# Performance work log

Measured on AMD Instinct MI355X. Metric: run time of the kernel, lower is better.

The kernel has to match this reference:

```python
import jax, jax.numpy as jnp
import numpy as np

I = 512   # input_size
H = 512   # hidden_size
Z = 0.1   # zoneout rate (eval-mode deterministic blend)
S = 128   # number of segments
B = 64    # batch


def setup_inputs() -> dict:
    rng = np.random.default_rng(0)
    durs = rng.integers(4, 13, size=(S, B)).astype(np.int64)  # [S, B], all >= 1
    T = int(durs.sum(0).max())
    key = jax.random.key(0)
    k0, k1, k2, k3, k4 = jax.random.split(key, 5)
    k = 1.0 / np.sqrt(H)
    x = jax.random.normal(k0, (T, B, I), jnp.float32)
    W_ih = jax.random.uniform(k1, (4 * H, I), jnp.float32, -k, k)
    W_hh = jax.random.uniform(k2, (4 * H, H), jnp.float32, -k, k)
    b_ih = jax.random.uniform(k3, (4 * H,), jnp.float32, -k, k)
    b_hh = jax.random.uniform(k4, (4 * H,), jnp.float32, -k, k)
    return {"x": x, "durs": jnp.asarray(durs), "W_ih": W_ih, "W_hh": W_hh,
            "b_ih": b_ih, "b_hh": b_hh}


def _duration_masks(durs, T):
    # durs: [S, B] -> per-batch segment-end (reset) frame indices and masks
    durs_bs = durs.T                                   # [B, S]
    reset_idx = jnp.cumsum(durs_bs, axis=1) - 1        # [B, S] last frame of each segment
    mel_lengths = jnp.sum(durs_bs, axis=1)             # [B]
    t = jnp.arange(T)
    reset_mask = jnp.any(t[None, :, None] == reset_idx[:, None, :], axis=-1)  # [B, T]
    valid = t[None, :] < mel_lengths[:, None]          # [B, T] frames within mel length
    retain = (~reset_mask) & valid                     # state kept where not reset/pad
    return reset_idx, retain.T, valid.T                # retain/valid as [T, B]


def reference(x, durs, W_ih, W_hh, b_ih, b_hh):
    T, Bb, _ = x.shape
    reset_idx, retain, valid = _duration_masks(durs, T)
    # Precompute the input contribution to the gates for all timesteps (one big GEMM)
    xg = jnp.einsum('tbi,gi->tbg', x, W_ih) + b_ih + b_hh   # [T, B, 4H]
    retain_f = retain.astype(x.dtype)                       # [T, B]

    def step(carry, inp):
        h, c = carry
        xg_t, retain_t = inp
        gates = xg_t + h @ W_hh.T                           # [B, 4H]
        i, f, g, o = jnp.split(gates, 4, axis=-1)           # torch LSTMCell order i,f,g,o
        i = jax.nn.sigmoid(i); f = jax.nn.sigmoid(f); o = jax.nn.sigmoid(o)
        g = jnp.tanh(g)
        c_new = f * c + i * g
        h_new = o * jnp.tanh(c_new)
        # eval-mode zoneout: deterministic blend with previous state
        h_z = Z * h + (1.0 - Z) * h_new
        c_z = Z * c + (1.0 - Z) * c_new
        m = retain_t[:, None]                               # zero state at segment resets / padding
        return (h_z * m, c_z * m), h_z

    h0 = jnp.zeros((Bb, H), x.dtype)
    (h, c), outputs = jax.lax.scan(step, (h0, h0), (xg, retain_f))
    outputs = outputs * valid[:, :, None].astype(outputs.dtype)  # [T, B, H]
    # segout: hidden state at each segment's last frame -> [B, S, H]
    segout = jnp.take_along_axis(outputs.transpose(1, 0, 2), reset_idx[:, :, None], axis=1)
    return outputs, h, c, segout
```

## Files before the change

### kernel.cpp

```cpp
#include <hip/hip_runtime.h>
#include <hip/hip_fp16.h>

#define IDIM 512
#define HDIM 512
#define NGATE 2048
#define SEGS 128
#define BATCH 64
#define ZK 0.1f

typedef _Float16 f16;
typedef _Float16 f16x8 __attribute__((ext_vector_type(8)));
typedef float f32x4 __attribute__((ext_vector_type(4)));

__device__ __forceinline__ void gload16(const void* g, void* l) {
  __builtin_amdgcn_global_load_lds((const __attribute__((address_space(1))) void*)g,
                                   (__attribute__((address_space(3))) void*)l, 16, 0, 0);
}
__device__ __forceinline__ float sigmoidf_(float x) { return 1.0f / (1.0f + __expf(-x)); }
__device__ __forceinline__ float tanhf_(float x) { return 2.0f / (1.0f + __expf(-2.0f * x)) - 1.0f; }

__global__ void prep_kernel(const int* __restrict__ durs, int4* __restrict__ meta,
                            int* __restrict__ Mk, int* __restrict__ mel) {
  __shared__ int hist[16];
  __shared__ int cur[16];
  int tid = threadIdx.x;
  if (tid < 16) hist[tid] = 0;
  __syncthreads();
  int b = tid;
  for (int s = 0; s < SEGS; ++s) {
    int d = durs[s * BATCH + b] & 15;
    atomicAdd(&hist[d], 1);
  }
  __syncthreads();
  if (tid == 0) {
    int run = 0;
    for (int d = 15; d >= 0; --d) { cur[d] = run; run += hist[d]; }
    for (int kk = 0; kk < 12; ++kk) Mk[kk] = cur[kk];
  }
  __syncthreads();
  int run = 0;
  for (int s = 0; s < SEGS; ++s) {
    int d = durs[s * BATCH + b] & 15;
    int pos = atomicAdd(&cur[d], 1);
    meta[pos] = make_int4(run, b, s, d);
    run += d;
  }
  mel[b] = run;
}

__global__ void wprep_kernel(const float* __restrict__ Wih, const float* __restrict__ Whh,
                             const float* __restrict__ bih, const float* __restrict__ bhh,
                             f16* __restrict__ Wc, float* __restrict__ biasp) {
  int n = blockIdx.x;
  int G = n >> 6, q = (n >> 4) & 3, r = n & 15;
  int j = G * 16 + r;
  int orig = q * 512 + j;
  for (int kk = threadIdx.x; kk < 1024; kk += blockDim.x) {
    float v = (kk < 512) ? Wih[(size_t)orig * 512 + kk] : Whh[(size_t)orig * 512 + kk - 512];
    Wc[(size_t)n * 1024 + kk] = (f16)v;
  }
  if (threadIdx.x == 0) biasp[n] = bih[orig] + bhh[orig];
}

__global__ void xconv_kernel(const float* __restrict__ x, f16* __restrict__ xh, long n8) {
  long i = (long)blockIdx.x * blockDim.x + threadIdx.x;
  long stride = (long)gridDim.x * blockDim.x;
  for (; i < n8; i += stride) {
    const float4* p = (const float4*)(x + i * 8);
    float4 a = p[0], bv = p[1];
    f16x8 o;
    o[0] = (f16)a.x;  o[1] = (f16)a.y;  o[2] = (f16)a.z;  o[3] = (f16)a.w;
    o[4] = (f16)bv.x; o[5] = (f16)bv.y; o[6] = (f16)bv.z; o[7] = (f16)bv.w;
    *(f16x8*)(xh + i * 8) = o;
  }
}

__global__ void zero_kernel(float* __restrict__ out, const int* __restrict__ mel, int T) {
  int bid = blockIdx.x;
  int tb = T * BATCH;
  if (bid < tb) {
    int t = bid / BATCH, b = bid - t * BATCH;
    if (t < mel[b]) return;
    float4* p = (float4*)(out + (size_t)bid * HDIM);
    p[threadIdx.x] = make_float4(0.f, 0.f, 0.f, 0.f);
  } else {
    int e = bid - tb;
    float4* p = (float4*)(out + (size_t)tb * HDIM + (size_t)e * HDIM);
    p[threadIdx.x] = make_float4(0.f, 0.f, 0.f, 0.f);
  }
}

template <bool FIRST>
__global__ __launch_bounds__(512, 1)
void step256_kernel(const f16* __restrict__ xh, const f16* __restrict__ Wc,
                    const float* __restrict__ biasp,
                    const f16* __restrict__ hprev, f16* __restrict__ hnext,
                    float* __restrict__ cst,
                    const int4* __restrict__ meta, const int* __restrict__ Mk,
                    float* __restrict__ out, int T, int k) {
  const int mk = Mk[k];
  const int nbx = gridDim.x;
  const int nwg = nbx * gridDim.y;
  const int orig = blockIdx.y * nbx + blockIdx.x;
  const int cpx = nwg >> 3;
  const int swz = (orig & 7) * cpx + (orig >> 3);
  const int by = swz / nbx, bx = swz - by * nbx;
  const int m0 = by * 256;
  if (m0 >= mk) return;
  const int n0 = bx * 256;

  __shared__ __align__(16) f16 As[2][256][64];
  __shared__ __align__(16) f16 Bs[2][256][64];
  __shared__ int4 metaS[256];

  const int tid = threadIdx.x;
  const int lane = tid & 63;
  const int w = tid >> 6;
  const int wr = w >> 2;
  const int wc = w & 3;
  const int lr = lane & 15;
  const int lk = lane >> 4;

  if (tid < 256) metaS[tid] = meta[m0 + tid];

  const int swzc = (((lane & 7) ^ ((lane >> 3) & 7)) << 3);
  size_t xoff[4];
  int ra4[4];
#pragma unroll
  for (int o = 0; o < 4; ++o) {
    int trow = o * 64 + w * 8 + (lane >> 3);
    int r = m0 + trow;
    int ra = (r < mk) ? r : 0;
    int4 mt = meta[ra];
    xoff[o] = ((size_t)(mt.x + k) * BATCH + mt.y) * IDIM + swzc;
    ra4[o] = ra;
  }

  auto stageA = [&](int o, int kb, int slot) {
    const f16* src;
    if (FIRST || kb < 8) src = xh + xoff[o] + kb * 64;
    else src = hprev + (size_t)ra4[o] * HDIM + (kb - 8) * 64 + swzc;
    gload16(src, &As[slot][o * 64 + w * 8][0]);
  };
  auto stageB = [&](int o, int kb, int slot) {
    int trow = o * 64 + w * 8 + (lane >> 3);
    gload16(Wc + (size_t)(n0 + trow) * 1024 + (size_t)kb * 64 + swzc,
            &Bs[slot][o * 64 + w * 8][0]);
  };

  auto lda = [&](int slot, int h, int f, int ks) -> f16x8 {
    int row = wr * 128 + h * 64 + f * 16 + lr;
    int ch = (((ks * 4 + lk) ^ (lr & 7)) << 3);
    return *(const f16x8*)&As[slot][row][ch];
  };
  auto ldb = [&](int slot, int q, int ks) -> f16x8 {
    int row = wc * 64 + q * 16 + lr;
    int ch = (((ks * 4 + lk) ^ (lr & 7)) << 3);
    return *(const f16x8*)&Bs[slot][row][ch];
  };

  f32x4 acc[8][4];
#pragma unroll
  for (int a = 0; a < 8; ++a)
#pragma unroll
    for (int bb = 0; bb < 4; ++bb) acc[a][bb] = (f32x4){0.f, 0.f, 0.f, 0.f};

  const int KB = FIRST ? 8 : 16;

#pragma unroll
  for (int o = 0; o < 4; ++o) stageA(o, 0, 0);
#pragma unroll
  for (int o = 0; o < 4; ++o) stageB(o, 0, 0);
#pragma unroll
  for (int o = 0; o < 4; ++o) stageA(o, 1, 1);
#pragma unroll
  for (int o = 0; o < 4; ++o) stageB(o, 1, 1);
  asm volatile("s_waitcnt vmcnt(8)" ::: "memory");
  __builtin_amdgcn_s_barrier();

  f16x8 aF[4][2], bF[4][2];

  for (int kt = 0; kt < KB; ++kt) {
    const int s = kt & 1;
    const bool st1 = (kt + 1 < KB);
    const bool st2 = (kt + 2 < KB);

#pragma unroll
    for (int f = 0; f < 4; ++f)
#pragma unroll
      for (int ks = 0; ks < 2; ++ks) aF[f][ks] = lda(s, 0, f, ks);
#pragma unroll
    for (int q = 0; q < 4; ++q)
#pragma unroll
      for (int ks = 0; ks < 2; ++ks) bF[q][ks] = ldb(s, q, ks);
    __builtin_amdgcn_s_barrier();
    __builtin_amdgcn_s_setprio(1);
#pragma unroll
    for (int f = 0; f < 4; ++f)
#pragma unroll
      for (int fn = 0; fn < 2; ++fn)
#pragma unroll
        for (int ks = 0; ks < 2; ++ks)
          acc[f][fn] = __builtin_amdgcn_mfma_f32_16x16x32_f16(aF[f][ks], bF[fn][ks], acc[f][fn], 0, 0, 0);
    __builtin_amdgcn_s_setprio(0);
    __builtin_amdgcn_s_barrier();

    if (st2) {
#pragma unroll
      for (int o = 0; o < 4; ++o) stageB(o, kt + 2, s);
    }
    __builtin_amdgcn_s_barrier();
    __builtin_amdgcn_s_setprio(1);
#pragma unroll
    for (int f = 0; f < 4; ++f)
#pragma unroll
      for (int fn = 2; fn < 4; ++fn)
#pragma unroll
        for (int ks = 0; ks < 2; ++ks)
          acc[f][fn] = __builtin_amdgcn_mfma_f32_16x16x32_f16(aF[f][ks], bF[fn][ks], acc[f][fn], 0, 0, 0);
    __builtin_amdgcn_s_setprio(0);
    __builtin_amdgcn_s_barrier();

#pragma unroll
    for (int f = 0; f < 4; ++f)
#pragma unroll
      for (int ks = 0; ks < 2; ++ks) aF[f][ks] = lda(s, 1, f, ks);
    if (st2) { stageA(0, kt + 2, s); stageA(2, kt + 2, s); }
    __builtin_amdgcn_s_barrier();
    __builtin_amdgcn_s_setprio(1);
#pragma unroll
    for (int f = 0; f < 4; ++f)
#pragma unroll
      for (int fn = 0; fn < 2; ++fn)
#pragma unroll
        for (int ks = 0; ks < 2; ++ks)
          acc[4 + f][fn] = __builtin_amdgcn_mfma_f32_16x16x32_f16(aF[f][ks], bF[fn][ks], acc[4 + f][fn], 0, 0, 0);
    __builtin_amdgcn_s_setprio(0);
    __builtin_amdgcn_s_barrier();

    if (st2) { stageA(1, kt + 2, s); stageA(3, kt + 2, s); }
    __builtin_amdgcn_s_setprio(1);
#pragma unroll
    for (int f = 0; f < 4; ++f)
#pragma unroll
      for (int fn = 2; fn < 4; ++fn)
#pragma unroll
        for (int ks = 0; ks < 2; ++ks)
          acc[4 + f][fn] = __builtin_amdgcn_mfma_f32_16x16x32_f16(aF[f][ks], bF[fn][ks], acc[4 + f][fn], 0, 0, 0);
    __builtin_amdgcn_s_setprio(0);
    if (st2) {
      asm volatile("s_waitcnt vmcnt(8)" ::: "memory");
    } else if (st1) {
      asm volatile("s_waitcnt vmcnt(0)" ::: "memory");
    }
    __builtin_amdgcn_s_barrier();
  }

  float bq[4];
#pragma unroll
  for (int q = 0; q < 4; ++q) bq[q] = biasp[n0 + wc * 64 + q * 16 + lr];
  const int j = ((n0 + wc * 64) >> 6) * 16 + lr;
  const size_t segoff = (size_t)T * BATCH * HDIM + (size_t)2 * BATCH * HDIM;

#pragma unroll
  for (int fm = 0; fm < 8; ++fm) {
#pragma unroll
    for (int reg = 0; reg < 4; ++reg) {
      int m = m0 + wr * 128 + fm * 16 + ((lane >> 4) << 2) + reg;
      if (m >= mk) continue;
      int4 mt = metaS[m - m0];
      float gi = acc[fm][0][reg] + bq[0];
      float gf = acc[fm][1][reg] + bq[1];
      float gg = acc[fm][2][reg] + bq[2];
      float go = acc[fm][3][reg] + bq[3];
      float iv = sigmoidf_(gi), fv = sigmoidf_(gf);
      float gv = tanhf_(gg), ov = sigmoidf_(go);
      float cp, hp;
      if (FIRST) { cp = 0.f; hp = 0.f; }
      else {
        cp = cst[(size_t)m * HDIM + j];
        hp = (float)hprev[(size_t)m * HDIM + j];
      }
      float cn = fv * cp + iv * gv;
      float hn = ov * tanhf_(cn);
      float hz = ZK * hp + (1.f - ZK) * hn;
      float cz = ZK * cp + (1.f - ZK) * cn;
      out[((size_t)(mt.x + k) * BATCH + mt.y) * HDIM + j] = hz;
      if (k == mt.w - 1) {
        out[segoff + ((size_t)mt.y * SEGS + mt.z) * HDIM + j] = hz;
      } else {
        hnext[(size_t)m * HDIM + j] = (f16)hz;
        cst[(size_t)m * HDIM + j] = cz;
      }
    }
  }
}

template <bool FIRST>
__global__ void step_kernel(const f16* __restrict__ xh, const f16* __restrict__ Wc,
                            const float* __restrict__ biasp,
                            const f16* __restrict__ hprev, f16* __restrict__ hnext,
                            float* __restrict__ cst,
                            const int4* __restrict__ meta, const int* __restrict__ Mk,
                            float* __restrict__ out, int T, int k) {
  const int mk = Mk[k];
  const int m0 = blockIdx.y * 128;
  if (m0 >= mk) return;
  const int n0 = blockIdx.x * 128;

  __shared__ __align__(16) f16 At[128][64];
  __shared__ __align__(16) f16 Bt[128][64];
  __shared__ int4 metaS[128];

  const int tid = threadIdx.x;
  const int lane = tid & 63;
  const int w = tid >> 6;
  const int wr = w >> 1, wc = w & 1;

  if (tid < 128) metaS[tid] = meta[m0 + tid];

  const f16* xsrc[4];
  const f16* hsrc[4];
  const f16* wsrc[4];
#pragma unroll
  for (int i = 0; i < 4; ++i) {
    int r = m0 + w * 32 + i * 8 + (lane >> 3);
    int ra = (r < mk) ? r : 0;
    int4 mt = meta[ra];
    xsrc[i] = xh + ((size_t)(mt.x + k) * BATCH + mt.y) * IDIM;
    hsrc[i] = hprev + (size_t)ra * HDIM;
    wsrc[i] = Wc + (size_t)(n0 + w * 32 + i * 8 + (lane >> 3)) * 1024;
  }
  const int koff = (lane & 7) * 8;

  f32x4 acc[4][4];
#pragma unroll
  for (int a = 0; a < 4; ++a)
#pragma unroll
    for (int bb = 0; bb < 4; ++bb) acc[a][bb] = (f32x4){0.f, 0.f, 0.f, 0.f};

  const int KB = FIRST ? 8 : 16;
  for (int kb = 0; kb < KB; ++kb) {
    __syncthreads();
#pragma unroll
    for (int i = 0; i < 4; ++i) {
      const f16* s;
      if (FIRST) s = xsrc[i] + kb * 64 + koff;
      else       s = (kb < 8) ? (xsrc[i] + kb * 64 + koff) : (hsrc[i] + (kb - 8) * 64 + koff);
      gload16(s, &At[w * 32 + i * 8][0]);
    }
#pragma unroll
    for (int i = 0; i < 4; ++i) gload16(wsrc[i] + kb * 64 + koff, &Bt[w * 32 + i * 8][0]);
    __syncthreads();

    const int lr = lane & 15;
    const int lk = (lane >> 4) * 8;
#pragma unroll
    for (int ks = 0; ks < 2; ++ks) {
      f16x8 af[4], bfr[4];
#pragma unroll
      for (int f = 0; f < 4; ++f) af[f] = *(const f16x8*)&At[wr * 64 + f * 16 + lr][ks * 32 + lk];
#pragma unroll
      for (int f = 0; f < 4; ++f) bfr[f] = *(const f16x8*)&Bt[wc * 64 + f * 16 + lr][ks * 32 + lk];
#pragma unroll
      for (int fm = 0; fm < 4; ++fm)
#pragma unroll
        for (int fn = 0; fn < 4; ++fn)
          acc[fm][fn] = __builtin_amdgcn_mfma_f32_16x16x32_f16(af[fm], bfr[fn], acc[fm][fn], 0, 0, 0);
    }
  }

  const int r15 = lane & 15;
  float bq[4];
#pragma unroll
  for (int q = 0; q < 4; ++q) bq[q] = biasp[n0 + wc * 64 + q * 16 + r15];
  const int j = ((n0 + wc * 64) >> 6) * 16 + r15;
  const size_t segoff = (size_t)T * BATCH * HDIM + (size_t)2 * BATCH * HDIM;

#pragma unroll
  for (int fm = 0; fm < 4; ++fm) {
#pragma unroll
    for (int reg = 0; reg < 4; ++reg) {
      int m = m0 + wr * 64 + fm * 16 + ((lane >> 4) << 2) + reg;
      if (m >= mk) continue;
      int4 mt = metaS[m - m0];
      float gi = acc[fm][0][reg] + bq[0];
      float gf = acc[fm][1][reg] + bq[1];
      float gg = acc[fm][2][reg] + bq[2];
      float go = acc[fm][3][reg] + bq[3];
      float iv = sigmoidf_(gi), fv = sigmoidf_(gf);
      float gv = tanhf_(gg), ov = sigmoidf_(go);
      float cp, hp;
      if (FIRST) { cp = 0.f; hp = 0.f; }
      else {
        cp = cst[(size_t)m * HDIM + j];
        hp = (float)hprev[(size_t)m * HDIM + j];
      }
      float cn = fv * cp + iv * gv;
      float hn = ov * tanhf_(cn);
      float hz = ZK * hp + (1.f - ZK) * hn;
      float cz = ZK * cp + (1.f - ZK) * cn;
      out[((size_t)(mt.x + k) * BATCH + mt.y) * HDIM + j] = hz;
      if (k == mt.w - 1) {
        out[segoff + ((size_t)mt.y * SEGS + mt.z) * HDIM + j] = hz;
      } else {
        hnext[(size_t)m * HDIM + j] = (f16)hz;
        cst[(size_t)m * HDIM + j] = cz;
      }
    }
  }
}

extern "C" void kernel_launch(void* const* d_in, const int* in_sizes, int n_in,
                              void* d_out, int out_size, void* d_ws, size_t ws_size,
                              hipStream_t stream) {
  const float* x = (const float*)d_in[0];
  const int* durs = (const int*)d_in[1];
  const float* Wih = (const float*)d_in[2];
  const float* Whh = (const float*)d_in[3];
  const float* bih = (const float*)d_in[4];
  const float* bhh = (const float*)d_in[5];
  float* out = (float*)d_out;
  const int T = in_sizes[0] / (BATCH * IDIM);

  char* ws = (char*)d_ws;
  size_t off = 0;
  auto alloc = [&](size_t bytes) {
    void* p = ws + off;
    off = (off + bytes + 255) & ~(size_t)255;
    return p;
  };
  f16* xh     = (f16*)alloc((size_t)T * BATCH * IDIM * 2);
  f16* Wc     = (f16*)alloc((size_t)NGATE * 1024 * 2);
  float* biasp= (float*)alloc((size_t)NGATE * 4);
  f16* hst0   = (f16*)alloc((size_t)SEGS * BATCH * HDIM * 2);
  f16* hst1   = (f16*)alloc((size_t)SEGS * BATCH * HDIM * 2);
  float* cst  = (float*)alloc((size_t)SEGS * BATCH * HDIM * 4);
  int4* meta  = (int4*)alloc((size_t)SEGS * BATCH * 16);
  int* Mk     = (int*)alloc(64);
  int* mel    = (int*)alloc(64);

  prep_kernel<<<1, 64, 0, stream>>>(durs, meta, Mk, mel);
  wprep_kernel<<<NGATE, 256, 0, stream>>>(Wih, Whh, bih, bhh, Wc, biasp);
  long n8 = (long)T * BATCH * IDIM / 8;
  xconv_kernel<<<2048, 256, 0, stream>>>(x, xh, n8);
  zero_kernel<<<T * BATCH + 128, 128, 0, stream>>>(out, mel, T);

  dim3 hgrid(8, 32);
  step256_kernel<true><<<hgrid, 512, 0, stream>>>(xh, Wc, biasp, hst0, hst1, cst, meta, Mk, out, T, 0);
  for (int k = 1; k < 8; ++k) {
    f16* hp = (k & 1) ? hst1 : hst0;
    f16* hn = (k & 1) ? hst0 : hst1;
    step256_kernel<false><<<hgrid, 512, 0, stream>>>(xh, Wc, biasp, hp, hn, cst, meta, Mk, out, T, k);
  }
  dim3 sgrid(16, 64);
  for (int k = 8; k < 12; ++k) {
    f16* hp = (k & 1) ? hst1 : hst0;
    f16* hn = (k & 1) ? hst0 : hst1;
    step_kernel<false><<<sgrid, 256, 0, stream>>>(xh, Wc, biasp, hp, hn, cst, meta, Mk, out, T, k);
  }
}
```

Before: 654.7 us.

## Fuse per-step LSTM launches into one persistent cooperative kernel with grid sync

Replaces the 12 separate step launches, which mixed 256-tile and 128-tile kernels, with a single cooperative persistent kernel of 256 blocks. The kernel loops over the 12 frame positions and calls grid.sync between them, and it always uses 256x256 tiles with a simple row-major tile mapping instead of the XCD swizzle. The zero kernel also becomes grid-stride with a fixed grid. The goal is to remove launch gaps and tail idle time between dependent steps. In exchange, the later small steps now use large tiles, which can leave many blocks idle, and the swizzle that spread tiles across XCDs for cache locality is gone.

```diff
diff --git a/kernel.cpp b/kernel.cpp
--- a/kernel.cpp
+++ b/kernel.cpp
@@ -1,5 +1,8 @@
 #include <hip/hip_runtime.h>
 #include <hip/hip_fp16.h>
+#include <hip/hip_cooperative_groups.h>
+
+namespace cg = cooperative_groups;
 
 #define IDIM 512
 #define HDIM 512
@@ -27,10 +30,7 @@
   if (tid < 16) hist[tid] = 0;
   __syncthreads();
   int b = tid;
-  for (int s = 0; s < SEGS; ++s) {
-    int d = durs[s * BATCH + b] & 15;
-    atomicAdd(&hist[d], 1);
-  }
+  for (int s = 0; s < SEGS; ++s) atomicAdd(&hist[durs[s * BATCH + b] & 15], 1);
   __syncthreads();
   if (tid == 0) {
     int run = 0;
@@ -75,44 +75,37 @@
   }
 }
 
-__global__ void zero_kernel(float* __restrict__ out, const int* __restrict__ mel, int T) {
-  int bid = blockIdx.x;
+__global__ void zero_kernel(float* __restrict__ out, const int* __restrict__ mel,
+                            int T, int total) {
   int tb = T * BATCH;
-  if (bid < tb) {
-    int t = bid / BATCH, b = bid - t * BATCH;
-    if (t < mel[b]) return;
-    float4* p = (float4*)(out + (size_t)bid * HDIM);
-    p[threadIdx.x] = make_float4(0.f, 0.f, 0.f, 0.f);
-  } else {
-    int e = bid - tb;
-    float4* p = (float4*)(out + (size_t)tb * HDIM + (size_t)e * HDIM);
-    p[threadIdx.x] = make_float4(0.f, 0.f, 0.f, 0.f);
-  }
-}
-
-template <bool FIRST>
+  for (int bid = blockIdx.x; bid < total; bid += gridDim.x) {
+    if (bid < tb) {
+      int t = bid / BATCH, b = bid - t * BATCH;
+      if (t < mel[b]) continue;
+      float4* p = (float4*)(out + (size_t)bid * HDIM);
+      p[threadIdx.x] = make_float4(0.f, 0.f, 0.f, 0.f);
+    } else {
+      int e = bid - tb;
+      float4* p = (float4*)(out + (size_t)tb * HDIM + (size_t)e * HDIM);
+      p[threadIdx.x] = make_float4(0.f, 0.f, 0.f, 0.f);
+    }
+  }
+}
+
 __global__ __launch_bounds__(512, 1)
-void step256_kernel(const f16* __restrict__ xh, const f16* __restrict__ Wc,
+void persist_kernel(const f16* __restrict__ xh, const f16* __restrict__ Wc,
                     const float* __restrict__ biasp,
-                    const f16* __restrict__ hprev, f16* __restrict__ hnext,
+                    f16* __restrict__ hst0, f16* __restrict__ hst1,
                     float* __restrict__ cst,
                     const int4* __restrict__ meta, const int* __restrict__ Mk,
-                    float* __restrict__ out, int T, int k) {
-  const int mk = Mk[k];
-  const int nbx = gridDim.x;
-  const int nwg = nbx * gridDim.y;
-  const int orig = blockIdx.y * nbx + blockIdx.x;
-  const int cpx = nwg >> 3;
-  const int swz = (orig & 7) * cpx + (orig >> 3);
-  const int by = swz / nbx, bx = swz - by * nbx;
-  const int m0 = by * 256;
-  if (m0 >= mk) return;
-  const int n0 = bx * 256;
+                    float* __restrict__ out, int T) {
+  cg::grid_group grid = cg::this_grid();
 
   __shared__ __align__(16) f16 As[2][256][64];
   __shared__ __align__(16) f16 Bs[2][256][64];
   __shared__ int4 metaS[256];
 
+  const int bid = blockIdx.x;
   const int tid = threadIdx.x;
   const int lane = tid & 63;
   const int w = tid >> 6;
@@ -120,294 +113,194 @@
   const int wc = w & 3;
   const int lr = lane & 15;
   const int lk = lane >> 4;
-
-  if (tid < 256) metaS[tid] = meta[m0 + tid];
-
   const int swzc = (((lane & 7) ^ ((lane >> 3) & 7)) << 3);
-  size_t xoff[4];
-  int ra4[4];
-#pragma unroll
-  for (int o = 0; o < 4; ++o) {
-    int trow = o * 64 + w * 8 + (lane >> 3);
-    int r = m0 + trow;
-    int ra = (r < mk) ? r : 0;
-    int4 mt = meta[ra];
-    xoff[o] = ((size_t)(mt.x + k) * BATCH + mt.y) * IDIM + swzc;
-    ra4[o] = ra;
-  }
-
-  auto stageA = [&](int o, int kb, int slot) {
-    const f16* src;
-    if (FIRST || kb < 8) src = xh + xoff[o] + kb * 64;
-    else src = hprev + (size_t)ra4[o] * HDIM + (kb - 8) * 64 + swzc;
-    gload16(src, &As[slot][o * 64 + w * 8][0]);
-  };
-  auto stageB = [&](int o, int kb, int slot) {
-    int trow = o * 64 + w * 8 + (lane >> 3);
-    gload16(Wc + (size_t)(n0 + trow) * 1024 + (size_t)kb * 64 + swzc,
-            &Bs[slot][o * 64 + w * 8][0]);
-  };
-
-  auto lda = [&](int slot, int h, int f, int ks) -> f16x8 {
-    int row = wr * 128 + h * 64 + f * 16 + lr;
-    int ch = (((ks * 4 + lk) ^ (lr & 7)) << 3);
-    return *(const f16x8*)&As[slot][row][ch];
-  };
-  auto ldb = [&](int slot, int q, int ks) -> f16x8 {
-    int row = wc * 64 + q * 16 + lr;
-    int ch = (((ks * 4 + lk) ^ (lr & 7)) << 3);
-    return *(const f16x8*)&Bs[slot][row][ch];
-  };
-
-  f32x4 acc[8][4];
-#pragma unroll
-  for (int a = 0; a < 8; ++a)
-#pragma unroll
-    for (int bb = 0; bb < 4; ++bb) acc[a][bb] = (f32x4){0.f, 0.f, 0.f, 0.f};
-
-  const int KB = FIRST ? 8 : 16;
-
-#pragma unroll
-  for (int o = 0; o < 4; ++o) stageA(o, 0, 0);
-#pragma unroll
-  for (int o = 0; o < 4; ++o) stageB(o, 0, 0);
-#pragma unroll
-  for (int o = 0; o < 4; ++o) stageA(o, 1, 1);
-#pragma unroll
-  for (int o = 0; o < 4; ++o) stageB(o, 1, 1);
-  asm volatile("s_waitcnt vmcnt(8)" ::: "memory");
-  __builtin_amdgcn_s_barrier();
-
-  f16x8 aF[4][2], bF[4][2];
-
-  for (int kt = 0; kt < KB; ++kt) {
-    const int s = kt & 1;
-    const bool st1 = (kt + 1 < KB);
-    const bool st2 = (kt + 2 < KB);
-
-#pragma unroll
-    for (int f = 0; f < 4; ++f)
-#pragma unroll
-      for (int ks = 0; ks < 2; ++ks) aF[f][ks] = lda(s, 0, f, ks);
-#pragma unroll
-    for (int q = 0; q < 4; ++q)
-#pragma unroll
-      for (int ks = 0; ks < 2; ++ks) bF[q][ks] = ldb(s, q, ks);
-    __builtin_amdgcn_s_barrier();
-    __builtin_amdgcn_s_setprio(1);
-#pragma unroll
-    for (int f = 0; f < 4; ++f)
-#pragma unroll
-      for (int fn = 0; fn < 2; ++fn)
-#pragma unroll
-        for (int ks = 0; ks < 2; ++ks)
-          acc[f][fn] = __builtin_amdgcn_mfma_f32_16x16x32_f16(aF[f][ks], bF[fn][ks], acc[f][fn], 0, 0, 0);
-    __builtin_amdgcn_s_setprio(0);
-    __builtin_amdgcn_s_barrier();
-
-    if (st2) {
-#pragma unroll
-      for (int o = 0; o < 4; ++o) stageB(o, kt + 2, s);
-    }
-    __builtin_amdgcn_s_barrier();
-    __builtin_amdgcn_s_setprio(1);
-#pragma unroll
-    for (int f = 0; f < 4; ++f)
-#pragma unroll
-      for (int fn = 2; fn < 4; ++fn)
-#pragma unroll
-        for (int ks = 0; ks < 2; ++ks)
-          acc[f][fn] = __builtin_amdgcn_mfma_f32_16x16x32_f16(aF[f][ks], bF[fn][ks], acc[f][fn], 0, 0, 0);
-    __builtin_amdgcn_s_setprio(0);
-    __builtin_amdgcn_s_barrier();
-
-#pragma unroll
-    for (int f = 0; f < 4; ++f)
-#pragma unroll
-      for (int ks = 0; ks < 2; ++ks) aF[f][ks] = lda(s, 1, f, ks);
-    if (st2) { stageA(0, kt + 2, s); stageA(2, kt + 2, s); }
-    __builtin_amdgcn_s_barrier();
-    __builtin_amdgcn_s_setprio(1);
-#pragma unroll
-    for (int f = 0; f < 4; ++f)
-#pragma unroll
-      for (int fn = 0; fn < 2; ++fn)
-#pragma unroll
-        for (int ks = 0; ks < 2; ++ks)
-          acc[4 + f][fn] = __builtin_amdgcn_mfma_f32_16x16x32_f16(aF[f][ks], bF[fn][ks], acc[4 + f][fn], 0, 0, 0);
-    __builtin_amdgcn_s_setprio(0);
-    __builtin_amdgcn_s_barrier();
-
-    if (st2) { stageA(1, kt + 2, s); stageA(3, kt + 2, s); }
-    __builtin_amdgcn_s_setprio(1);
-#pragma unroll
-    for (int f = 0; f < 4; ++f)
-#pragma unroll
-      for (int fn = 2; fn < 4; ++fn)
-#pragma unroll
-        for (int ks = 0; ks < 2; ++ks)
-          acc[4 + f][fn] = __builtin_amdgcn_mfma_f32_16x16x32_f16(aF[f][ks], bF[fn][ks], acc[4 + f][fn], 0, 0, 0);
-    __builtin_amdgcn_s_setprio(0);
-    if (st2) {
+  const size_t segoff = (size_t)T * BATCH * HDIM + (size_t)2 * BATCH * HDIM;
+
+  for (int k = 0; k < 12; ++k) {
+    const int mk = Mk[k];
+    const int npan = (mk + 255) >> 8;
+    const int ntiles = npan * 8;
+    const f16* hprev = (k & 1) ? hst1 : hst0;
+    f16* hnext = (k & 1) ? hst0 : hst1;
+
+    if (bid < ntiles) {
+      const int by = bid >> 3, bx = bid & 7;
+      const int m0 = by * 256;
+      const int n0 = bx * 256;
+
+      if (tid < 256) metaS[tid] = meta[m0 + tid];
+
+      size_t xoff[4];
+      int ra4[4];
+#pragma unroll
+      for (int o = 0; o < 4; ++o) {
+        int trow = o * 64 + w * 8 + (lane >> 3);
+        int r = m0 + trow;
+        int ra = (r < mk) ? r : 0;
+        int4 mt = meta[ra];
+        xoff[o] = ((size_t)(mt.x + k) * BATCH + mt.y) * IDIM + swzc;
+        ra4[o] = ra;
+      }
+
+      auto stageA = [&](int o, int kb, int slot) {
+        const f16* src;
+        if (k == 0 || kb < 8) src = xh + xoff[o] + kb * 64;
+        else src = hprev + (size_t)ra4[o] * HDIM + (kb - 8) * 64 + swzc;
+        gload16(src, &As[slot][o * 64 + w * 8][0]);
+      };
+      auto stageB = [&](int o, int kb, int slot) {
+        int trow = o * 64 + w * 8 + (lane >> 3);
+        gload16(Wc + (size_t)(n0 + trow) * 1024 + (size_t)kb * 64 + swzc,
+                &Bs[slot][o * 64 + w * 8][0]);
+      };
+      auto lda = [&](int slot, int h, int f, int ks) -> f16x8 {
+        int row = wr * 128 + h * 64 + f * 16 + lr;
+        int ch = (((ks * 4 + lk) ^ (lr & 7)) << 3);
+        return *(const f16x8*)&As[slot][row][ch];
+      };
+      auto ldb = [&](int slot, int q, int ks) -> f16x8 {
+        int row = wc * 64 + q * 16 + lr;
+        int ch = (((ks * 4 + lk) ^ (lr & 7)) << 3);
+        return *(const f16x8*)&Bs[slot][row][ch];
+      };
+
+      f32x4 acc[8][4];
+#pragma unroll
+      for (int a = 0; a < 8; ++a)
+#pragma unroll
+        for (int bb = 0; bb < 4; ++bb) acc[a][bb] = (f32x4){0.f, 0.f, 0.f, 0.f};
+
+      const int KB = (k == 0) ? 8 : 16;
+
+#pragma unroll
+      for (int o = 0; o < 4; ++o) stageA(o, 0, 0);
+#pragma unroll
+      for (int o = 0; o < 4; ++o) stageB(o, 0, 0);
+#pragma unroll
+      for (int o = 0; o < 4; ++o) stageA(o, 1, 1);
+#pragma unroll
+      for (int o = 0; o < 4; ++o) stageB(o, 1, 1);
       asm volatile("s_waitcnt vmcnt(8)" ::: "memory");
-    } else if (st1) {
-      asm volatile("s_waitcnt vmcnt(0)" ::: "memory");
-    }
-    __builtin_amdgcn_s_barrier();
-  }
-
-  float bq[4];
-#pragma unroll
-  for (int q = 0; q < 4; ++q) bq[q] = biasp[n0 + wc * 64 + q * 16 + lr];
-  const int j = ((n0 + wc * 64) >> 6) * 16 + lr;
-  const size_t segoff = (size_t)T * BATCH * HDIM + (size_t)2 * BATCH * HDIM;
-
-#pragma unroll
-  for (int fm = 0; fm < 8; ++fm) {
-#pragma unroll
-    for (int reg = 0; reg < 4; ++reg) {
-      int m = m0 + wr * 128 + fm * 16 + ((lane >> 4) << 2) + reg;
-      if (m >= mk) continue;
-      int4 mt = metaS[m - m0];
-      float gi = acc[fm][0][reg] + bq[0];
-      float gf = acc[fm][1][reg] + bq[1];
-      float gg = acc[fm][2][reg] + bq[2];
-      float go = acc[fm][3][reg] + bq[3];
-      float iv = sigmoidf_(gi), fv = sigmoidf_(gf);
-      float gv = tanhf_(gg), ov = sigmoidf_(go);
-      float cp, hp;
-      if (FIRST) { cp = 0.f; hp = 0.f; }
-      else {
-        cp = cst[(size_t)m * HDIM + j];
-        hp = (float)hprev[(size_t)m * HDIM + j];
+      __builtin_amdgcn_s_barrier();
+
+      f16x8 aF[4][2], bF[4][2];
+
+      for (int kt = 0; kt < KB; ++kt) {
+        const int s = kt & 1;
+        const bool st1 = (kt + 1 < KB);
+        const bool st2 = (kt + 2 < KB);
+
+#pragma unroll
+        for (int f = 0; f < 4; ++f)
+#pragma unroll
+          for (int ks = 0; ks < 2; ++ks) aF[f][ks] = lda(s, 0, f, ks);
+#pragma unroll
+        for (int q = 0; q < 4; ++q)
+#pragma unroll
+          for (int ks = 0; ks < 2; ++ks) bF[q][ks] = ldb(s, q, ks);
+        __builtin_amdgcn_s_barrier();
+        __builtin_amdgcn_s_setprio(1);
+#pragma unroll
+        for (int f = 0; f < 4; ++f)
+#pragma unroll
+          for (int fn = 0; fn < 2; ++fn)
+#pragma unroll
+            for (int ks = 0; ks < 2; ++ks)
+              acc[f][fn] = __builtin_amdgcn_mfma_f32_16x16x32_f16(aF[f][ks], bF[fn][ks], acc[f][fn], 0, 0, 0);
+        __builtin_amdgcn_s_setprio(0);
+        __builtin_amdgcn_s_barrier();
+
+        if (st2) {
+#pragma unroll
+          for (int o = 0; o < 4; ++o) stageB(o, kt + 2, s);
+        }
+        __builtin_amdgcn_s_barrier();
+        __builtin_amdgcn_s_setprio(1);
+#pragma unroll
+        for (int f = 0; f < 4; ++f)
+#pragma unroll
+          for (int fn = 2; fn < 4; ++fn)
+#pragma unroll
+            for (int ks = 0; ks < 2; ++ks)
+              acc[f][fn] = __builtin_amdgcn_mfma_f32_16x16x32_f16(aF[f][ks], bF[fn][ks], acc[f][fn], 0, 0, 0);
+        __builtin_amdgcn_s_setprio(0);
+        __builtin_amdgcn_s_barrier();
+
+#pragma unroll
+        for (int f = 0; f < 4; ++f)
+#pragma unroll
+          for (int ks = 0; ks < 2; ++ks) aF[f][ks] = lda(s, 1, f, ks);
+        if (st2) { stageA(0, kt + 2, s); stageA(2, kt + 2, s); }
+        __builtin_amdgcn_s_barrier();
+        __builtin_amdgcn_s_setprio(1);
+#pragma unroll
+        for (int f = 0; f < 4; ++f)
+#pragma unroll
+          for (int fn = 0; fn < 2; ++fn)
+#pragma unroll
+            for (int ks = 0; ks < 2; ++ks)
+              acc[4 + f][fn] = __builtin_amdgcn_mfma_f32_16x16x32_f16(aF[f][ks], bF[fn][ks], acc[4 + f][fn], 0, 0, 0);
+        __builtin_amdgcn_s_setprio(0);
+        __builtin_amdgcn_s_barrier();
+
+        if (st2) { stageA(1, kt + 2, s); stageA(3, kt + 2, s); }
+        __builtin_amdgcn_s_setprio(1);
+#pragma unroll
+        for (int f = 0; f < 4; ++f)
+#pragma unroll
+          for (int fn = 2; fn < 4; ++fn)
+#pragma unroll
+            for (int ks = 0; ks < 2; ++ks)
+              acc[4 + f][fn] = __builtin_amdgcn_mfma_f32_16x16x32_f16(aF[f][ks], bF[fn][ks], acc[4 + f][fn], 0, 0, 0);
+        __builtin_amdgcn_s_setprio(0);
+        if (st2) {
+          asm volatile("s_waitcnt vmcnt(8)" ::: "memory");
+        } else if (st1) {
+          asm volatile("s_waitcnt vmcnt(0)" ::: "memory");
+        }
+        __builtin_amdgcn_s_barrier();
       }
-      float cn = fv * cp + iv * gv;
-      float hn = ov * tanhf_(cn);
-      float hz = ZK * hp + (1.f - ZK) * hn;
-      float cz = ZK * cp + (1.f - ZK) * cn;
-      out[((size_t)(mt.x + k) * BATCH + mt.y) * HDIM + j] = hz;
-      if (k == mt.w - 1) {
-        out[segoff + ((size_t)mt.y * SEGS + mt.z) * HDIM + j] = hz;
-      } else {
-        hnext[(size_t)m * HDIM + j] = (f16)hz;
-        cst[(size_t)m * HDIM + j] = cz;
+
+      float bq[4];
+#pragma unroll
+      for (int q = 0; q < 4; ++q) bq[q] = biasp[n0 + wc * 64 + q * 16 + lr];
+      const int j = ((n0 + wc * 64) >> 6) * 16 + lr;
+
+#pragma unroll
+      for (int fm = 0; fm < 8; ++fm) {
+#pragma unroll
+        for (int reg = 0; reg < 4; ++reg) {
+          int m = m0 + wr * 128 + fm * 16 + ((lane >> 4) << 2) + reg;
+          if (m >= mk) continue;
+          int4 mt = metaS[m - m0];
+          float gi = acc[fm][0][reg] + bq[0];
+          float gf = acc[fm][1][reg] + bq[1];
+          float gg = acc[fm][2][reg] + bq[2];
+          float go = acc[fm][3][reg] + bq[3];
+          float iv = sigmoidf_(gi), fv = sigmoidf_(gf);
+          float gv = tanhf_(gg), ov = sigmoidf_(go);
+          float cp, hp;
+          if (k == 0) { cp = 0.f; hp = 0.f; }
+          else {
+            cp = cst[(size_t)m * HDIM + j];
+            hp = (float)hprev[(size_t)m * HDIM + j];
+          }
+          float cn = fv * cp + iv * gv;
+          float hn = ov * tanhf_(cn);
+          float hz = ZK * hp + (1.f - ZK) * hn;
+          float cz = ZK * cp + (1.f - ZK) * cn;
+          out[((size_t)(mt.x + k) * BATCH + mt.y) * HDIM + j] = hz;
+          if (k == mt.w - 1) {
+            out[segoff + ((size_t)mt.y * SEGS + mt.z) * HDIM + j] = hz;
+          } else {
+            hnext[(size_t)m * HDIM + j] = (f16)hz;
+            cst[(size_t)m * HDIM + j] = cz;
+          }
+        }
       }
     }
-  }
-}
-
-template <bool FIRST>
-__global__ void step_kernel(const f16* __restrict__ xh, const f16* __restrict__ Wc,
-                            const float* __restrict__ biasp,
-                            const f16* __restrict__ hprev, f16* __restrict__ hnext,
-                            float* __restrict__ cst,
-                            const int4* __restrict__ meta, const int* __restrict__ Mk,
-                            float* __restrict__ out, int T, int k) {
-  const int mk = Mk[k];
-  const int m0 = blockIdx.y * 128;
-  if (m0 >= mk) return;
-  const int n0 = blockIdx.x * 128;
-
-  __shared__ __align__(16) f16 At[128][64];
-  __shared__ __align__(16) f16 Bt[128][64];
-  __shared__ int4 metaS[128];
-
-  const int tid = threadIdx.x;
-  const int lane = tid & 63;
-  const int w = tid >> 6;
-  const int wr = w >> 1, wc = w & 1;
-
-  if (tid < 128) metaS[tid] = meta[m0 + tid];
-
-  const f16* xsrc[4];
-  const f16* hsrc[4];
-  const f16* wsrc[4];
-#pragma unroll
-  for (int i = 0; i < 4; ++i) {
-    int r = m0 + w * 32 + i * 8 + (lane >> 3);
-    int ra = (r < mk) ? r : 0;
-    int4 mt = meta[ra];
-    xsrc[i] = xh + ((size_t)(mt.x + k) * BATCH + mt.y) * IDIM;
-    hsrc[i] = hprev + (size_t)ra * HDIM;
-    wsrc[i] = Wc + (size_t)(n0 + w * 32 + i * 8 + (lane >> 3)) * 1024;
-  }
-  const int koff = (lane & 7) * 8;
-
-  f32x4 acc[4][4];
-#pragma unroll
-  for (int a = 0; a < 4; ++a)
-#pragma unroll
-    for (int bb = 0; bb < 4; ++bb) acc[a][bb] = (f32x4){0.f, 0.f, 0.f, 0.f};
-
-  const int KB = FIRST ? 8 : 16;
-  for (int kb = 0; kb < KB; ++kb) {
-    __syncthreads();
-#pragma unroll
-    for (int i = 0; i < 4; ++i) {
-      const f16* s;
-      if (FIRST) s = xsrc[i] + kb * 64 + koff;
-      else       s = (kb < 8) ? (xsrc[i] + kb * 64 + koff) : (hsrc[i] + (kb - 8) * 64 + koff);
-      gload16(s, &At[w * 32 + i * 8][0]);
-    }
-#pragma unroll
-    for (int i = 0; i < 4; ++i) gload16(wsrc[i] + kb * 64 + koff, &Bt[w * 32 + i * 8][0]);
-    __syncthreads();
-
-    const int lr = lane & 15;
-    const int lk = (lane >> 4) * 8;
-#pragma unroll
-    for (int ks = 0; ks < 2; ++ks) {
-      f16x8 af[4], bfr[4];
-#pragma unroll
-      for (int f = 0; f < 4; ++f) af[f] = *(const f16x8*)&At[wr * 64 + f * 16 + lr][ks * 32 + lk];
-#pragma unroll
-      for (int f = 0; f < 4; ++f) bfr[f] = *(const f16x8*)&Bt[wc * 64 + f * 16 + lr][ks * 32 + lk];
-#pragma unroll
-      for (int fm = 0; fm < 4; ++fm)
-#pragma unroll
-        for (int fn = 0; fn < 4; ++fn)
-          acc[fm][fn] = __builtin_amdgcn_mfma_f32_16x16x32_f16(af[fm], bfr[fn], acc[fm][fn], 0, 0, 0);
-    }
-  }
-
-  const int r15 = lane & 15;
-  float bq[4];
-#pragma unroll
-  for (int q = 0; q < 4; ++q) bq[q] = biasp[n0 + wc * 64 + q * 16 + r15];
-  const int j = ((n0 + wc * 64) >> 6) * 16 + r15;
-  const size_t segoff = (size_t)T * BATCH * HDIM + (size_t)2 * BATCH * HDIM;
-
-#pragma unroll
-  for (int fm = 0; fm < 4; ++fm) {
-#pragma unroll
-    for (int reg = 0; reg < 4; ++reg) {
-      int m = m0 + wr * 64 + fm * 16 + ((lane >> 4) << 2) + reg;
-      if (m >= mk) continue;
-      int4 mt = metaS[m - m0];
-      float gi = acc[fm][0][reg] + bq[0];
-      float gf = acc[fm][1][reg] + bq[1];
-      float gg = acc[fm][2][reg] + bq[2];
-      float go = acc[fm][3][reg] + bq[3];
-      float iv = sigmoidf_(gi), fv = sigmoidf_(gf);
-      float gv = tanhf_(gg), ov = sigmoidf_(go);
-      float cp, hp;
-      if (FIRST) { cp = 0.f; hp = 0.f; }
-      else {
-        cp = cst[(size_t)m * HDIM + j];
-        hp = (float)hprev[(size_t)m * HDIM + j];
-      }
-      float cn = fv * cp + iv * gv;
-      float hn = ov * tanhf_(cn);
-      float hz = ZK * hp + (1.f - ZK) * hn;
-      float cz = ZK * cp + (1.f - ZK) * cn;
-      out[((size_t)(mt.x + k) * BATCH + mt.y) * HDIM + j] = hz;
-      if (k == mt.w - 1) {
-        out[segoff + ((size_t)mt.y * SEGS + mt.z) * HDIM + j] = hz;
-      } else {
-        hnext[(size_t)m * HDIM + j] = (f16)hz;
-        cst[(size_t)m * HDIM + j] = cz;
-      }
-    }
+
+    if (k < 11) grid.sync();
   }
 }
 
@@ -421,7 +314,7 @@
   const float* bih = (const float*)d_in[4];
   const float* bhh = (const float*)d_in[5];
   float* out = (float*)d_out;
-  const int T = in_sizes[0] / (BATCH * IDIM);
+  int T = in_sizes[0] / (BATCH * IDIM);
 
   char* ws = (char*)d_ws;
   size_t off = 0;
@@ -444,19 +337,10 @@
   wprep_kernel<<<NGATE, 256, 0, stream>>>(Wih, Whh, bih, bhh, Wc, biasp);
   long n8 = (long)T * BATCH * IDIM / 8;
   xconv_kernel<<<2048, 256, 0, stream>>>(x, xh, n8);
-  zero_kernel<<<T * BATCH + 128, 128, 0, stream>>>(out, mel, T);
-
-  dim3 hgrid(8, 32);
-  step256_kernel<true><<<hgrid, 512, 0, stream>>>(xh, Wc, biasp, hst0, hst1, cst, meta, Mk, out, T, 0);
-  for (int k = 1; k < 8; ++k) {
-    f16* hp = (k & 1) ? hst1 : hst0;
-    f16* hn = (k & 1) ? hst0 : hst1;
-    step256_kernel<false><<<hgrid, 512, 0, stream>>>(xh, Wc, biasp, hp, hn, cst, meta, Mk, out, T, k);
-  }
-  dim3 sgrid(16, 64);
-  for (int k = 8; k < 12; ++k) {
-    f16* hp = (k & 1) ? hst1 : hst0;
-    f16* hn = (k & 1) ? hst0 : hst1;
-    step_kernel<false><<<sgrid, 256, 0, stream>>>(xh, Wc, biasp, hp, hn, cst, meta, Mk, out, T, k);
-  }
-}
+  zero_kernel<<<2048, 128, 0, stream>>>(out, mel, T, T * BATCH + 128);
+
+  void* kargs[] = {(void*)&xh, (void*)&Wc, (void*)&biasp, (void*)&hst0, (void*)&hst1,
+                   (void*)&cst, (void*)&meta, (void*)&Mk, (void*)&out, (void*)&T};
+  hipLaunchCooperativeKernel((const void*)persist_kernel, dim3(256), dim3(512),
+                             kargs, 0, stream);
+}
```

After: 1.708 ms. +160.9%, slower.

## Restructure step GEMM main loop into two-tile unrolled pipeline with fragment prefetch

Applied to the files above, without the earlier changes.

Unrolls the step256 main loop over two K-tiles per iteration. It splits the A and B LDS fragment reads into quarters that are prefetched one MFMA block ahead, and reorders the staging of the next tiles with finer vmcnt waits, so LDS reads and global loads overlap more with MFMA work. The zero kernel also becomes a grid-stride loop with a fixed 2048-block grid instead of one block per row. In exchange the kernel holds more live fragment registers and depends on a more fragile wait and barrier schedule.

```diff
diff --git a/kernel.cpp b/kernel.cpp
--- a/kernel.cpp
+++ b/kernel.cpp
@@ -27,10 +27,7 @@
   if (tid < 16) hist[tid] = 0;
   __syncthreads();
   int b = tid;
-  for (int s = 0; s < SEGS; ++s) {
-    int d = durs[s * BATCH + b] & 15;
-    atomicAdd(&hist[d], 1);
-  }
+  for (int s = 0; s < SEGS; ++s) atomicAdd(&hist[durs[s * BATCH + b] & 15], 1);
   __syncthreads();
   if (tid == 0) {
     int run = 0;
@@ -75,18 +72,20 @@
   }
 }
 
-__global__ void zero_kernel(float* __restrict__ out, const int* __restrict__ mel, int T) {
-  int bid = blockIdx.x;
+__global__ void zero_kernel(float* __restrict__ out, const int* __restrict__ mel,
+                            int T, int total) {
   int tb = T * BATCH;
-  if (bid < tb) {
-    int t = bid / BATCH, b = bid - t * BATCH;
-    if (t < mel[b]) return;
-    float4* p = (float4*)(out + (size_t)bid * HDIM);
-    p[threadIdx.x] = make_float4(0.f, 0.f, 0.f, 0.f);
-  } else {
-    int e = bid - tb;
-    float4* p = (float4*)(out + (size_t)tb * HDIM + (size_t)e * HDIM);
-    p[threadIdx.x] = make_float4(0.f, 0.f, 0.f, 0.f);
+  for (int bid = blockIdx.x; bid < total; bid += gridDim.x) {
+    if (bid < tb) {
+      int t = bid / BATCH, b = bid - t * BATCH;
+      if (t < mel[b]) continue;
+      float4* p = (float4*)(out + (size_t)bid * HDIM);
+      p[threadIdx.x] = make_float4(0.f, 0.f, 0.f, 0.f);
+    } else {
+      int e = bid - tb;
+      float4* p = (float4*)(out + (size_t)tb * HDIM + (size_t)e * HDIM);
+      p[threadIdx.x] = make_float4(0.f, 0.f, 0.f, 0.f);
+    }
   }
 }
 
@@ -100,10 +99,8 @@
                     float* __restrict__ out, int T, int k) {
   const int mk = Mk[k];
   const int nbx = gridDim.x;
-  const int nwg = nbx * gridDim.y;
   const int orig = blockIdx.y * nbx + blockIdx.x;
-  const int cpx = nwg >> 3;
-  const int swz = (orig & 7) * cpx + (orig >> 3);
+  const int swz = (orig & 7) * 32 + (orig >> 3);
   const int by = swz / nbx, bx = swz - by * nbx;
   const int m0 = by * 256;
   if (m0 >= mk) return;
@@ -147,7 +144,6 @@
     gload16(Wc + (size_t)(n0 + trow) * 1024 + (size_t)kb * 64 + swzc,
             &Bs[slot][o * 64 + w * 8][0]);
   };
-
   auto lda = [&](int slot, int h, int f, int ks) -> f16x8 {
     int row = wr * 128 + h * 64 + f * 16 + lr;
     int ch = (((ks * 4 + lk) ^ (lr & 7)) << 3);
@@ -166,6 +162,7 @@
     for (int bb = 0; bb < 4; ++bb) acc[a][bb] = (f32x4){0.f, 0.f, 0.f, 0.f};
 
   const int KB = FIRST ? 8 : 16;
+  const int NITER = KB >> 1;
 
 #pragma unroll
   for (int o = 0; o < 4; ++o) stageA(o, 0, 0);
@@ -178,83 +175,118 @@
   asm volatile("s_waitcnt vmcnt(8)" ::: "memory");
   __builtin_amdgcn_s_barrier();
 
-  f16x8 aF[4][2], bF[4][2];
-
-  for (int kt = 0; kt < KB; ++kt) {
-    const int s = kt & 1;
-    const bool st1 = (kt + 1 < KB);
-    const bool st2 = (kt + 2 < KB);
+  f16x8 aF0[4][2], aF1[4][2], aN0[4][2], aN1[4][2];
+  f16x8 bA[2][2], bB[2][2], bC[2][2], bD[2][2];
+
+#pragma unroll
+  for (int f = 0; f < 4; ++f)
+#pragma unroll
+    for (int ks = 0; ks < 2; ++ks) aF0[f][ks] = lda(0, 0, f, ks);
+#pragma unroll
+  for (int q = 0; q < 2; ++q)
+#pragma unroll
+    for (int ks = 0; ks < 2; ++ks) bA[q][ks] = ldb(0, q, ks);
+
+#define MFMA_Q(ACC_R, ACC_C, AFR, BFR)                                              \
+  __builtin_amdgcn_s_setprio(1);                                                    \
+  _Pragma("unroll") for (int f = 0; f < 4; ++f)                                     \
+    _Pragma("unroll") for (int q = 0; q < 2; ++q)                                   \
+      _Pragma("unroll") for (int ks = 0; ks < 2; ++ks)                              \
+        acc[ACC_R + f][ACC_C + q] =                                                 \
+            __builtin_amdgcn_mfma_f32_16x16x32_f16(AFR[f][ks], BFR[q][ks],          \
+                                                   acc[ACC_R + f][ACC_C + q], 0, 0, 0); \
+  __builtin_amdgcn_s_setprio(0);
+
+  for (int i = 0; i < NITER; ++i) {
+    const int kt0 = 2 * i;
+    const bool st = (i + 1 < NITER);
+
+#pragma unroll
+    for (int q = 0; q < 2; ++q)
+#pragma unroll
+      for (int ks = 0; ks < 2; ++ks) bB[q][ks] = ldb(0, q + 2, ks);
+    __builtin_amdgcn_s_barrier();
+    MFMA_Q(0, 0, aF0, bA)
+    __builtin_amdgcn_s_barrier();
 
 #pragma unroll
     for (int f = 0; f < 4; ++f)
 #pragma unroll
-      for (int ks = 0; ks < 2; ++ks) aF[f][ks] = lda(s, 0, f, ks);
-#pragma unroll
-    for (int q = 0; q < 4; ++q)
-#pragma unroll
-      for (int ks = 0; ks < 2; ++ks) bF[q][ks] = ldb(s, q, ks);
-    __builtin_amdgcn_s_barrier();
-    __builtin_amdgcn_s_setprio(1);
+      for (int ks = 0; ks < 2; ++ks) aF1[f][ks] = lda(0, 1, f, ks);
+    if (st) {
+#pragma unroll
+      for (int o = 0; o < 4; ++o) stageB(o, kt0 + 2, 0);
+    }
+    __builtin_amdgcn_s_barrier();
+    MFMA_Q(0, 2, aF0, bB)
+    if (st) { asm volatile("s_waitcnt vmcnt(4)" ::: "memory"); }
+    else    { asm volatile("s_waitcnt vmcnt(0)" ::: "memory"); }
+    __builtin_amdgcn_s_barrier();
+
+    if (st) {
+#pragma unroll
+      for (int o = 0; o < 4; ++o) stageA(o, kt0 + 2, 0);
+    }
+    __builtin_amdgcn_s_barrier();
+    MFMA_Q(4, 0, aF1, bA)
+    __builtin_amdgcn_s_barrier();
+
 #pragma unroll
     for (int f = 0; f < 4; ++f)
 #pragma unroll
-      for (int fn = 0; fn < 2; ++fn)
-#pragma unroll
-        for (int ks = 0; ks < 2; ++ks)
-          acc[f][fn] = __builtin_amdgcn_mfma_f32_16x16x32_f16(aF[f][ks], bF[fn][ks], acc[f][fn], 0, 0, 0);
-    __builtin_amdgcn_s_setprio(0);
-    __builtin_amdgcn_s_barrier();
-
-    if (st2) {
-#pragma unroll
-      for (int o = 0; o < 4; ++o) stageB(o, kt + 2, s);
-    }
-    __builtin_amdgcn_s_barrier();
-    __builtin_amdgcn_s_setprio(1);
+      for (int ks = 0; ks < 2; ++ks) aN0[f][ks] = lda(1, 0, f, ks);
+#pragma unroll
+    for (int q = 0; q < 2; ++q)
+#pragma unroll
+      for (int ks = 0; ks < 2; ++ks) bC[q][ks] = ldb(1, q, ks);
+    __builtin_amdgcn_s_barrier();
+    MFMA_Q(4, 2, aF1, bB)
+    __builtin_amdgcn_s_barrier();
+
+#pragma unroll
+    for (int q = 0; q < 2; ++q)
+#pragma unroll
+      for (int ks = 0; ks < 2; ++ks) bD[q][ks] = ldb(1, q + 2, ks);
+    __builtin_amdgcn_s_barrier();
+    MFMA_Q(0, 0, aN0, bC)
+    __builtin_amdgcn_s_barrier();
+
 #pragma unroll
     for (int f = 0; f < 4; ++f)
 #pragma unroll
-      for (int fn = 2; fn < 4; ++fn)
-#pragma unroll
-        for (int ks = 0; ks < 2; ++ks)
-          acc[f][fn] = __builtin_amdgcn_mfma_f32_16x16x32_f16(aF[f][ks], bF[fn][ks], acc[f][fn], 0, 0, 0);
-    __builtin_amdgcn_s_setprio(0);
-    __builtin_amdgcn_s_barrier();
-
-#pragma unroll
-    for (int f = 0; f < 4; ++f)
-#pragma unroll
-      for (int ks = 0; ks < 2; ++ks) aF[f][ks] = lda(s, 1, f, ks);
-    if (st2) { stageA(0, kt + 2, s); stageA(2, kt + 2, s); }
-    __builtin_amdgcn_s_barrier();
-    __builtin_amdgcn_s_setprio(1);
-#pragma unroll
-    for (int f = 0; f < 4; ++f)
-#pragma unroll
-      for (int fn = 0; fn < 2; ++fn)
-#pragma unroll
-        for (int ks = 0; ks < 2; ++ks)
-          acc[4 + f][fn] = __builtin_amdgcn_mfma_f32_16x16x32_f16(aF[f][ks], bF[fn][ks], acc[4 + f][fn], 0, 0, 0);
-    __builtin_amdgcn_s_setprio(0);
-    __builtin_amdgcn_s_barrier();
-
-    if (st2) { stageA(1, kt + 2, s); stageA(3, kt + 2, s); }
-    __builtin_amdgcn_s_setprio(1);
-#pragma unroll
-    for (int f = 0; f < 4; ++f)
-#pragma unroll
-      for (int fn = 2; fn < 4; ++fn)
-#pragma unroll
-        for (int ks = 0; ks < 2; ++ks)
-          acc[4 + f][fn] = __builtin_amdgcn_mfma_f32_16x16x32_f16(aF[f][ks], bF[fn][ks], acc[4 + f][fn], 0, 0, 0);
-    __builtin_amdgcn_s_setprio(0);
-    if (st2) {
-      asm volatile("s_waitcnt vmcnt(8)" ::: "memory");
-    } else if (st1) {
-      asm volatile("s_waitcnt vmcnt(0)" ::: "memory");
-    }
-    __builtin_amdgcn_s_barrier();
-  }
+      for (int ks = 0; ks < 2; ++ks) aN1[f][ks] = lda(1, 1, f, ks);
+    if (st) {
+#pragma unroll
+      for (int o = 0; o < 4; ++o) stageB(o, kt0 + 3, 1);
+    }
+    __builtin_amdgcn_s_barrier();
+    MFMA_Q(0, 2, aN0, bD)
+    if (st) { asm volatile("s_waitcnt vmcnt(4)" ::: "memory"); }
+    __builtin_amdgcn_s_barrier();
+
+    if (st) {
+#pragma unroll
+      for (int o = 0; o < 4; ++o) stageA(o, kt0 + 3, 1);
+    }
+    __builtin_amdgcn_s_barrier();
+    MFMA_Q(4, 0, aN1, bC)
+    __builtin_amdgcn_s_barrier();
+
+    if (st) {
+#pragma unroll
+      for (int f = 0; f < 4; ++f)
+#pragma unroll
+        for (int ks = 0; ks < 2; ++ks) aF0[f][ks] = lda(0, 0, f, ks);
+#pragma unroll
+      for (int q = 0; q < 2; ++q)
+#pragma unroll
+        for (int ks = 0; ks < 2; ++ks) bA[q][ks] = ldb(0, q, ks);
+    }
+    __builtin_amdgcn_s_barrier();
+    MFMA_Q(4, 2, aN1, bD)
+    __builtin_amdgcn_s_barrier();
+  }
+#undef MFMA_Q
 
   float bq[4];
 #pragma unroll
@@ -444,7 +476,7 @@
   wprep_kernel<<<NGATE, 256, 0, stream>>>(Wih, Whh, bih, bhh, Wc, biasp);
   long n8 = (long)T * BATCH * IDIM / 8;
   xconv_kernel<<<2048, 256, 0, stream>>>(x, xh, n8);
-  zero_kernel<<<T * BATCH + 128, 128, 0, stream>>>(out, mel, T);
+  zero_kernel<<<2048, 128, 0, stream>>>(out, mel, T, T * BATCH + 128);
 
   dim3 hgrid(8, 32);
   step256_kernel<true><<<hgrid, 512, 0, stream>>>(xh, Wc, biasp, hst0, hst1, cst, meta, Mk, out, T, 0);
```

After: 1.013 ms. 54.8% more time.
